# Optimization experiments

Measured on AMD Instinct MI355X. Metric: run time of the kernel, lower is better.

## Reference

```python
import jax, jax.numpy as jnp
import numpy as np

B, S, D = 2, 2048, 1024
H, E = 16, 64          # n_heads, head_dim
DFF = 4096             # intermediate
R_ATTN, R_OUT, R_FF = 32, 512, 512
LN_EPS = 1e-5
SCALE = 1.0 / np.sqrt(E)


def setup_inputs() -> dict:
    key = jax.random.key(0)
    ks = jax.random.split(key, 24)
    s = 0.02
    inp = {
        "hidden_states": jax.random.normal(ks[0], (B, S, D), jnp.float32),
        "ln1_w": jnp.ones((D,), jnp.float32),
        "ln1_b": jnp.zeros((D,), jnp.float32),
        "q_U": jax.random.normal(ks[1], (H, E, R_ATTN), jnp.float32) * s,
        "q_V": jax.random.normal(ks[2], (H, R_ATTN, D), jnp.float32) * s,
        "q_bias": jax.random.normal(ks[3], (H, E), jnp.float32) * s,
        "k_U": jax.random.normal(ks[4], (H, E, R_ATTN), jnp.float32) * s,
        "k_V": jax.random.normal(ks[5], (H, R_ATTN, D), jnp.float32) * s,
        "k_bias": jax.random.normal(ks[6], (H, E), jnp.float32) * s,
        "v_U": jax.random.normal(ks[7], (H, E, R_ATTN), jnp.float32) * s,
        "v_V": jax.random.normal(ks[8], (H, R_ATTN, D), jnp.float32) * s,
        "v_bias": jax.random.normal(ks[9], (H, E), jnp.float32) * s,
        "out_U": jax.random.normal(ks[10], (D, R_OUT), jnp.float32) * s,
        "out_V": jax.random.normal(ks[11], (R_OUT, D), jnp.float32) * s,
        "out_bias": jnp.zeros((D,), jnp.float32),
        "ln2_w": jnp.ones((D,), jnp.float32),
        "ln2_b": jnp.zeros((D,), jnp.float32),
        "fc1_U": jax.random.normal(ks[12], (DFF, R_FF), jnp.float32) * s,
        "fc1_V": jax.random.normal(ks[13], (R_FF, D), jnp.float32) * s,
        "fc1_bias": jnp.zeros((DFF,), jnp.float32),
        "fc2_U": jax.random.normal(ks[14], (D, R_FF), jnp.float32) * s,
        "fc2_V": jax.random.normal(ks[15], (R_FF, DFF), jnp.float32) * s,
        "fc2_bias": jnp.zeros((D,), jnp.float32),
    }
    return inp


def _layernorm(x, w, b):
    mu = jnp.mean(x, axis=-1, keepdims=True)
    var = jnp.mean(jnp.square(x - mu), axis=-1, keepdims=True)
    return (x - mu) * jax.lax.rsqrt(var + LN_EPS) * w + b


def _per_head_svd(x, U, V, bias):
    # x: [b,s,d]; V: [h,r,d]; U: [h,e,r]; bias: [h,e] -> [b,h,s,e]
    t = jnp.einsum("bsd,hrd->bhsr", x, V)
    return jnp.einsum("bhsr,her->bhse", t, U) + bias[None, :, None, :]


def reference(hidden_states, ln1_w, ln1_b, q_U, q_V, q_bias, k_U, k_V, k_bias,
              v_U, v_V, v_bias, out_U, out_V, out_bias, ln2_w, ln2_b,
              fc1_U, fc1_V, fc1_bias, fc2_U, fc2_V, fc2_bias):
    b, s, d = hidden_states.shape
    normed = _layernorm(hidden_states, ln1_w, ln1_b)

    q = _per_head_svd(normed, q_U, q_V, q_bias)  # [b,h,s,e]
    k = _per_head_svd(normed, k_U, k_V, k_bias)
    v = _per_head_svd(normed, v_U, v_V, v_bias)

    scores = jnp.einsum("bhqe,bhke->bhqk", q, k) * SCALE
    causal = jnp.tril(jnp.ones((s, s), dtype=bool))
    scores = jnp.where(causal, scores, -jnp.inf)
    probs = jax.nn.softmax(scores, axis=-1)
    attn = jnp.einsum("bhqk,bhke->bhqe", probs, v)
    attn = attn.transpose(0, 2, 1, 3).reshape(b, s, d)  # [b,s,d]

    attn = jnp.einsum("bsr,dr->bsd", jnp.einsum("bsd,rd->bsr", attn, out_V), out_U) + out_bias
    hidden_states = hidden_states + attn

    normed = _layernorm(hidden_states, ln2_w, ln2_b)
    ff = jnp.einsum("bsr,fr->bsf", jnp.einsum("bsd,rd->bsr", normed, fc1_V), fc1_U) + fc1_bias
    ff = jax.nn.gelu(ff, approximate=False)  # exact erf gelu as in torch F.gelu
    ff = jnp.einsum("bsr,dr->bsd", jnp.einsum("bsf,rf->bsr", ff, fc2_V), fc2_U) + fc2_bias
    hidden_states = hidden_states + ff
    return (hidden_states,)
```

## Files before the change

### kernel.cpp

```cpp
#include <hip/hip_runtime.h>
#include <hip/hip_bf16.h>
#include <math.h>

#define Bc 2
#define Sc 2048
#define Dc 1024
#define Hc 16
#define Ec 64
#define DFFc 4096
#define SCALEc 0.125f
#define SCLOG2E 0.18033688f
#define LN_EPSc 1e-5f
#define BH_STRIDE 131072

typedef short bf16x8 __attribute__((ext_vector_type(8)));
typedef unsigned short u16x4 __attribute__((ext_vector_type(4)));
typedef unsigned short u16x8 __attribute__((ext_vector_type(8)));
typedef float f32x4 __attribute__((ext_vector_type(4)));
typedef float f32x16 __attribute__((ext_vector_type(16)));
typedef unsigned int u32x4 __attribute__((ext_vector_type(4)));
#define MFMA16(a, b, c) __builtin_amdgcn_mfma_f32_16x16x32_bf16(a, b, c, 0, 0, 0)
#define MFMA32(a, b, c) __builtin_amdgcn_mfma_f32_32x32x16_bf16(a, b, c, 0, 0, 0)
#define GLDS16(g, l)                                                            \
  __builtin_amdgcn_global_load_lds((const __attribute__((address_space(1))) void*)(g), \
                                   (__attribute__((address_space(3))) void*)(l), 16, 0, 0)

static __device__ __forceinline__ unsigned short f2bf(float x) {
  unsigned u = __float_as_uint(x);
  unsigned r = (u + 0x7FFFu + ((u >> 16) & 1u)) >> 16;
  return (unsigned short)r;
}
static __device__ __forceinline__ unsigned cvtpk(float lo, float hi) {
  unsigned r;
  asm("v_cvt_pk_bf16_f32 %0, %1, %2" : "=v"(r) : "v"(lo), "v"(hi));
  return r;
}

__global__ __launch_bounds__(256) void prep(
    const float* __restrict__ s3, const float* __restrict__ s4, const float* __restrict__ s5,
    const float* __restrict__ s6, const float* __restrict__ s7, const float* __restrict__ s8,
    unsigned short* __restrict__ wsu,
    const float* __restrict__ x, const float* __restrict__ lw, const float* __restrict__ lb,
    unsigned short* __restrict__ nout,
    const float* __restrict__ qB, const float* __restrict__ kB, const float* __restrict__ vB,
    float* __restrict__ biasF) {
  __shared__ float sm[8];
  int tid = threadIdx.x;
  if (blockIdx.x < 6144) {
    int i = (blockIdx.x * 256 + tid) * 4;
    const float* s;
    int off;
    if (i < 1572864) {
      int seg = i >> 19;
      off = i & 524287;
      s = (seg == 0) ? s3 : (seg == 1) ? s4 : s5;
    } else if (i < 3670016) { s = s6; off = i - 1572864; }
    else if (i < 5767168)   { s = s7; off = i - 3670016; }
    else                    { s = s8; off = i - 5767168; }
    float4 v = *(const float4*)(s + off);
    u16x4 o = {f2bf(v.x), f2bf(v.y), f2bf(v.z), f2bf(v.w)};
    *(u16x4*)(wsu + 1572864 + i) = o;
    return;
  }
  if (blockIdx.x >= 6144 + 4096) {
    int k = blockIdx.x - 6144 - 4096;
    const float* src = (k == 0) ? qB : (k == 1) ? kB : vB;
    float sc = (k == 0) ? SCLOG2E : 1.0f;
    int i = tid * 4;
    float4 v = *(const float4*)(src + i);
    float4 o = {v.x * sc, v.y * sc, v.z * sc, v.w * sc};
    *(float4*)(biasF + k * 1024 + i) = o;
    return;
  }
  int row = blockIdx.x - 6144;
  const float* xr = x + (size_t)row * Dc;
  float v[4];
  float sum = 0.f;
#pragma unroll
  for (int i = 0; i < 4; ++i) { v[i] = xr[tid + i * 256]; sum += v[i]; }
#pragma unroll
  for (int off = 32; off > 0; off >>= 1) sum += __shfl_down(sum, off, 64);
  if ((tid & 63) == 0) sm[tid >> 6] = sum;
  __syncthreads();
  float mean = (sm[0] + sm[1] + sm[2] + sm[3]) * (1.f / Dc);
  float var = 0.f;
#pragma unroll
  for (int i = 0; i < 4; ++i) { float d0 = v[i] - mean; var += d0 * d0; }
#pragma unroll
  for (int off = 32; off > 0; off >>= 1) var += __shfl_down(var, off, 64);
  if ((tid & 63) == 0) sm[4 + (tid >> 6)] = var;
  __syncthreads();
  float rstd = rsqrtf((sm[4] + sm[5] + sm[6] + sm[7]) * (1.f / Dc) + LN_EPSc);
  unsigned short* orow = nout + (size_t)row * Dc;
#pragma unroll
  for (int i = 0; i < 4; ++i) {
    int c = tid + i * 256;
    orow[c] = f2bf((v[i] - mean) * rstd * lw[c] + lb[c]);
  }
}

__global__ __launch_bounds__(256) void makew(const float* __restrict__ qU,
                                             const float* __restrict__ kU,
                                             const float* __restrict__ vU,
                                             const float* __restrict__ qV,
                                             const float* __restrict__ kV,
                                             const float* __restrict__ vV,
                                             unsigned short* __restrict__ W) {
  int bid = blockIdx.x;
  int kind = bid >> 8;
  int h = (bid >> 4) & 15;
  int dblk = bid & 15;
  const float* U = (kind == 0) ? qU : (kind == 1) ? kU : vU;
  const float* V = (kind == 0) ? qV : (kind == 1) ? kV : vV;
  __shared__ float Us[64][33];
  __shared__ float Vs[32][64];
  int tid = threadIdx.x;
  for (int i = tid; i < 2048; i += 256) Us[i >> 5][i & 31] = U[h * 2048 + i];
  for (int i = tid; i < 2048; i += 256) {
    int r = i >> 6, d = i & 63;
    Vs[r][d] = V[h * 32768 + r * 1024 + dblk * 64 + d];
  }
  __syncthreads();
  int e = tid & 63;
  int dq = tid >> 6;
  float scale = (kind == 0) ? SCLOG2E : 1.0f;
  float acc[16] = {};
  for (int r = 0; r < 32; ++r) {
    float u = Us[e][r];
#pragma unroll
    for (int j = 0; j < 16; ++j) acc[j] += u * Vs[r][dq * 16 + j];
  }
  u16x8 o0, o1;
#pragma unroll
  for (int j = 0; j < 8; ++j) {
    o0[j] = f2bf(acc[j] * scale);
    o1[j] = f2bf(acc[8 + j] * scale);
  }
  size_t base = ((size_t)(kind * 1024 + h * 64 + e)) * 1024 + dblk * 64 + dq * 16;
  *(u16x8*)(W + base) = o0;
  *(u16x8*)(W + base + 8) = o1;
}

__global__ __launch_bounds__(256) void ln_bf16(const float* __restrict__ x,
                                               const float* __restrict__ w,
                                               const float* __restrict__ b,
                                               unsigned short* __restrict__ out) {
  __shared__ float sm[8];
  int row = blockIdx.x;
  int tid = threadIdx.x;
  const float* xr = x + (size_t)row * Dc;
  float v[4];
  float sum = 0.f;
#pragma unroll
  for (int i = 0; i < 4; ++i) { v[i] = xr[tid + i * 256]; sum += v[i]; }
#pragma unroll
  for (int off = 32; off > 0; off >>= 1) sum += __shfl_down(sum, off, 64);
  if ((tid & 63) == 0) sm[tid >> 6] = sum;
  __syncthreads();
  float mean = (sm[0] + sm[1] + sm[2] + sm[3]) * (1.f / Dc);
  float var = 0.f;
#pragma unroll
  for (int i = 0; i < 4; ++i) { float d0 = v[i] - mean; var += d0 * d0; }
#pragma unroll
  for (int off = 32; off > 0; off >>= 1) var += __shfl_down(var, off, 64);
  if ((tid & 63) == 0) sm[4 + (tid >> 6)] = var;
  __syncthreads();
  float rstd = rsqrtf((sm[4] + sm[5] + sm[6] + sm[7]) * (1.f / Dc) + LN_EPSc);
  unsigned short* orow = out + (size_t)row * Dc;
#pragma unroll
  for (int i = 0; i < 4; ++i) {
    int c = tid + i * 256;
    orow[c] = f2bf((v[i] - mean) * rstd * w[c] + b[c]);
  }
}

template <int BM, int BN>
__global__ __launch_bounds__(256) void gemm_bf16(const unsigned short* __restrict__ A,
                                                 const unsigned short* __restrict__ W,
                                                 float* __restrict__ Cf,
                                                 unsigned short* __restrict__ Cb,
                                                 const float* __restrict__ bias,
                                                 const float* __restrict__ res,
                                                 int M, int N, int K, int gelu, int nbm) {
  constexpr int BK = 64;
  constexpr int MT = BM / 32;
  constexpr int NT = BN / 32;
  __shared__ unsigned short As[2][BM * BK];
  __shared__ unsigned short Bs[2][BN * BK];
  int tid = threadIdx.x;
  int lane = tid & 63;
  int wid = tid >> 6;
  int cl = lane & 15, grp = lane >> 4;
  int wr = wid >> 1, wc = wid & 1;
  int bm = blockIdx.x % nbm;
  int bn = blockIdx.x / nbm;
  const unsigned short* Ab = A + (size_t)(bm * BM) * K;
  const unsigned short* Wb = W + (size_t)(bn * BN) * K;
  f32x4 acc[MT][NT];
  f32x4 z4 = {0.f, 0.f, 0.f, 0.f};
#pragma unroll
  for (int i = 0; i < MT; ++i)
#pragma unroll
    for (int j = 0; j < NT; ++j) acc[i][j] = z4;
  int r0 = tid >> 3;
  int c0 = (tid & 7) * 8;

#define STAGE(buf, k0)                                                         \
  {                                                                            \
    _Pragma("unroll") for (int l = 0; l < BM / 32; ++l) {                      \
      int row = r0 + l * 32;                                                   \
      int sc = c0 ^ ((row & 7) * 8);                                           \
      GLDS16(Ab + (size_t)row * K + (k0) + sc, &As[buf][(tid + l * 256) * 8]); \
    }                                                                          \
    _Pragma("unroll") for (int l = 0; l < BN / 32; ++l) {                      \
      int row = r0 + l * 32;                                                   \
      int sc = c0 ^ ((row & 7) * 8);                                           \
      GLDS16(Wb + (size_t)row * K + (k0) + sc, &Bs[buf][(tid + l * 256) * 8]); \
    }                                                                          \
  }

  int nt = K / BK;
  STAGE(0, 0)
  __syncthreads();
  for (int t = 0; t < nt; ++t) {
    int cur = t & 1;
    if (t + 1 < nt) STAGE(cur ^ 1, (t + 1) * BK)
#pragma unroll
    for (int kk = 0; kk < 2; ++kk) {
      bf16x8 af[MT], bfr[NT];
#pragma unroll
      for (int i = 0; i < MT; ++i) {
        int row = wr * (BM / 2) + i * 16 + cl;
        af[i] = *(const bf16x8*)&As[cur][row * BK + ((kk * 32 + grp * 8) ^ ((row & 7) * 8))];
      }
#pragma unroll
      for (int j = 0; j < NT; ++j) {
        int row = wc * (BN / 2) + j * 16 + cl;
        bfr[j] = *(const bf16x8*)&Bs[cur][row * BK + ((kk * 32 + grp * 8) ^ ((row & 7) * 8))];
      }
#pragma unroll
      for (int i = 0; i < MT; ++i)
#pragma unroll
        for (int j = 0; j < NT; ++j) acc[i][j] = MFMA16(af[i], bfr[j], acc[i][j]);
    }
    __syncthreads();
  }
#undef STAGE

#pragma unroll
  for (int i = 0; i < MT; ++i) {
    int row = bm * BM + wr * (BM / 2) + i * 16 + grp * 4;
#pragma unroll
    for (int j = 0; j < NT; ++j) {
      int col = bn * BN + wc * (BN / 2) + j * 16 + cl;
      float bv = bias ? bias[col] : 0.f;
#pragma unroll
      for (int r = 0; r < 4; ++r) {
        float v = acc[i][j][r] + bv;
        if (gelu) v = 0.5f * v * (1.f + erff(v * 0.70710678118f));
        if (res) v += res[(size_t)(row + r) * N + col];
        if (Cb) Cb[(size_t)(row + r) * N + col] = f2bf(v);
        else Cf[(size_t)(row + r) * N + col] = v;
      }
    }
  }
}

__global__ __launch_bounds__(256) void gemm_qkv(const unsigned short* __restrict__ A,
                                                const unsigned short* __restrict__ W,
                                                const float* __restrict__ bias,
                                                unsigned short* __restrict__ qO,
                                                unsigned short* __restrict__ kO,
                                                unsigned short* __restrict__ vO,
                                                int K, int nbm) {
  constexpr int BM = 128, BN = 64, BK = 64;
  constexpr int MT = BM / 32;
  constexpr int NT = BN / 32;
  const int N = 3072;
  __shared__ unsigned short As[2][BM * BK];
  __shared__ unsigned short Bs[2][BN * BK];
  int tid = threadIdx.x;
  int lane = tid & 63;
  int wid = tid >> 6;
  int cl = lane & 15, grp = lane >> 4;
  int wr = wid >> 1, wc = wid & 1;
  int bm = blockIdx.x % nbm;
  int bn = blockIdx.x / nbm;
  const unsigned short* Ab = A + (size_t)(bm * BM) * K;
  const unsigned short* Wb = W + (size_t)(bn * BN) * K;
  f32x4 acc[MT][NT];
  f32x4 z4 = {0.f, 0.f, 0.f, 0.f};
#pragma unroll
  for (int i = 0; i < MT; ++i)
#pragma unroll
    for (int j = 0; j < NT; ++j) acc[i][j] = z4;
  int r0 = tid >> 3;
  int c0 = (tid & 7) * 8;

#define STAGE(buf, k0)                                                         \
  {                                                                            \
    _Pragma("unroll") for (int l = 0; l < BM / 32; ++l) {                      \
      int row = r0 + l * 32;                                                   \
      int sc = c0 ^ ((row & 7) * 8);                                           \
      GLDS16(Ab + (size_t)row * K + (k0) + sc, &As[buf][(tid + l * 256) * 8]); \
    }                                                                          \
    _Pragma("unroll") for (int l = 0; l < BN / 32; ++l) {                      \
      int row = r0 + l * 32;                                                   \
      int sc = c0 ^ ((row & 7) * 8);                                           \
      GLDS16(Wb + (size_t)row * K + (k0) + sc, &Bs[buf][(tid + l * 256) * 8]); \
    }                                                                          \
  }

  int nt = K / BK;
  STAGE(0, 0)
  __syncthreads();
  for (int t = 0; t < nt; ++t) {
    int cur = t & 1;
    if (t + 1 < nt) STAGE(cur ^ 1, (t + 1) * BK)
#pragma unroll
    for (int kk = 0; kk < 2; ++kk) {
      bf16x8 af[MT], bfr[NT];
#pragma unroll
      for (int i = 0; i < MT; ++i) {
        int row = wr * (BM / 2) + i * 16 + cl;
        af[i] = *(const bf16x8*)&As[cur][row * BK + ((kk * 32 + grp * 8) ^ ((row & 7) * 8))];
      }
#pragma unroll
      for (int j = 0; j < NT; ++j) {
        int row = wc * (BN / 2) + j * 16 + cl;
        bfr[j] = *(const bf16x8*)&Bs[cur][row * BK + ((kk * 32 + grp * 8) ^ ((row & 7) * 8))];
      }
#pragma unroll
      for (int i = 0; i < MT; ++i)
#pragma unroll
        for (int j = 0; j < NT; ++j) acc[i][j] = MFMA16(af[i], bfr[j], acc[i][j]);
    }
    __syncthreads();
  }
#undef STAGE

#pragma unroll
  for (int i = 0; i < MT; ++i) {
    int row0 = bm * BM + wr * (BM / 2) + i * 16 + grp * 4;
#pragma unroll
    for (int j = 0; j < NT; ++j) {
      int col = bn * BN + wc * (BN / 2) + j * 16 + cl;
      float bv = bias[col];
      int kind = col >> 10;
      int c1 = col & 1023;
      int h = c1 >> 6;
      int e = c1 & 63;
#pragma unroll
      for (int r = 0; r < 4; ++r) {
        int row = row0 + r;
        unsigned short hv = f2bf(acc[i][j][r] + bv);
        int b = row >> 11;
        int rs = row & 2047;
        int sb = rs >> 5;
        int bh = b * Hc + h;
        if (kind < 2) {
          int s = rs & 31;
          int ec = e >> 3;
          int jj = e & 7;
          int es = ec >> 1, hi2 = ec & 1;
          int lanep = s + hi2 * 32;
          unsigned short* out = (kind == 0) ? qO : kO;
          out[(size_t)bh * BH_STRIDE + (size_t)((sb * 4 + es) * 64 + lanep) * 8 + jj] = hv;
        } else {
          int within = rs & 31;
          int sg = within >> 3;
          int si = within & 7;
          int eo = e >> 5, llp = e & 31;
          int h2 = sg >> 1, hi2 = sg & 1;
          int ix = eo * 2 + h2;
          int lanep = llp + hi2 * 32;
          vO[(size_t)bh * BH_STRIDE + (size_t)((sb * 4 + ix) * 64 + lanep) * 8 + si] = hv;
        }
      }
    }
  }
}

template <int BM, int BN>
__global__ __launch_bounds__(256) void gemm_splitk2(const unsigned short* __restrict__ A,
                                                    const unsigned short* __restrict__ W,
                                                    float* __restrict__ P0,
                                                    float* __restrict__ P1,
                                                    int M, int N, int K, int nbm) {
  constexpr int BK = 64;
  constexpr int MT = BM / 32;
  constexpr int NT = BN / 32;
  __shared__ unsigned short As[2][BM * BK];
  __shared__ unsigned short Bs[2][BN * BK];
  int tid = threadIdx.x;
  int lane = tid & 63;
  int wid = tid >> 6;
  int cl = lane & 15, grp = lane >> 4;
  int wr = wid >> 1, wc = wid & 1;
  int per = nbm * (N / BN);
  int slice = blockIdx.x / per;
  int inner = blockIdx.x % per;
  int bm = inner % nbm;
  int bn = inner / nbm;
  int Ks = K / 2;
  const unsigned short* Ab = A + (size_t)(bm * BM) * K + (size_t)slice * Ks;
  const unsigned short* Wb = W + (size_t)(bn * BN) * K + (size_t)slice * Ks;
  float* P = slice ? P1 : P0;
  f32x4 acc[MT][NT];
  f32x4 z4 = {0.f, 0.f, 0.f, 0.f};
#pragma unroll
  for (int i = 0; i < MT; ++i)
#pragma unroll
    for (int j = 0; j < NT; ++j) acc[i][j] = z4;
  int r0 = tid >> 3;
  int c0 = (tid & 7) * 8;

#define STAGE(buf, k0)                                                         \
  {                                                                            \
    _Pragma("unroll") for (int l = 0; l < BM / 32; ++l) {                      \
      int row = r0 + l * 32;                                                   \
      int sc = c0 ^ ((row & 7) * 8);                                           \
      GLDS16(Ab + (size_t)row * K + (k0) + sc, &As[buf][(tid + l * 256) * 8]); \
    }                                                                          \
    _Pragma("unroll") for (int l = 0; l < BN / 32; ++l) {                      \
      int row = r0 + l * 32;                                                   \
      int sc = c0 ^ ((row & 7) * 8);                                           \
      GLDS16(Wb + (size_t)row * K + (k0) + sc, &Bs[buf][(tid + l * 256) * 8]); \
    }                                                                          \
  }

  int nt = Ks / BK;
  STAGE(0, 0)
  __syncthreads();
  for (int t = 0; t < nt; ++t) {
    int cur = t & 1;
    if (t + 1 < nt) STAGE(cur ^ 1, (t + 1) * BK)
#pragma unroll
    for (int kk = 0; kk < 2; ++kk) {
      bf16x8 af[MT], bfr[NT];
#pragma unroll
      for (int i = 0; i < MT; ++i) {
        int row = wr * (BM / 2) + i * 16 + cl;
        af[i] = *(const bf16x8*)&As[cur][row * BK + ((kk * 32 + grp * 8) ^ ((row & 7) * 8))];
      }
#pragma unroll
      for (int j = 0; j < NT; ++j) {
        int row = wc * (BN / 2) + j * 16 + cl;
        bfr[j] = *(const bf16x8*)&Bs[cur][row * BK + ((kk * 32 + grp * 8) ^ ((row & 7) * 8))];
      }
#pragma unroll
      for (int i = 0; i < MT; ++i)
#pragma unroll
        for (int j = 0; j < NT; ++j) acc[i][j] = MFMA16(af[i], bfr[j], acc[i][j]);
    }
    __syncthreads();
  }
#undef STAGE

#pragma unroll
  for (int i = 0; i < MT; ++i) {
    int row = bm * BM + wr * (BM / 2) + i * 16 + grp * 4;
#pragma unroll
    for (int j = 0; j < NT; ++j) {
      int col = bn * BN + wc * (BN / 2) + j * 16 + cl;
#pragma unroll
      for (int r = 0; r < 4; ++r)
        P[(size_t)(row + r) * N + col] = acc[i][j][r];
    }
  }
}

__global__ __launch_bounds__(256) void reduce2(const float* __restrict__ P0,
                                               const float* __restrict__ P1,
                                               unsigned short* __restrict__ out, int n) {
  int i = (blockIdx.x * 256 + threadIdx.x) * 4;
  if (i >= n) return;
  float4 a = *(const float4*)(P0 + i);
  float4 b = *(const float4*)(P1 + i);
  u16x4 o = {f2bf(a.x + b.x), f2bf(a.y + b.y), f2bf(a.z + b.z), f2bf(a.w + b.w)};
  *(u16x4*)(out + i) = o;
}

__global__ __launch_bounds__(256) void attn_mfma(const unsigned short* __restrict__ qf_,
                                                 const unsigned short* __restrict__ kf_,
                                                 const unsigned short* __restrict__ vf_,
                                                 unsigned short* __restrict__ out) {
  __shared__ float MS[2][33][64];
  int tid = threadIdx.x;
  int wid = tid >> 6;
  int lane = tid & 63;
  int ll = lane & 31;
  int hi = lane >> 5;
  int bid = blockIdx.x;
  int xcd = bid & 7;
  int idx = bid >> 3;
  int qt = 63 - (idx >> 2);
  int bh = xcd + 8 * (idx & 3);
  int b = bh >> 4, h = bh & 15;
  const unsigned short* qb = qf_ + (size_t)bh * BH_STRIDE;
  const unsigned short* kb = kf_ + (size_t)bh * BH_STRIDE;
  const unsigned short* vb = vf_ + (size_t)bh * BH_STRIDE;
  int q0 = qt * 32;
  int nt = qt + 1;
  int full = nt - 1;
  int fs = wid * full / 4;
  int fe = (wid + 1) * full / 4;

  bf16x8 qf[4];
#pragma unroll
  for (int es = 0; es < 4; ++es)
    qf[es] = *(const bf16x8*)(qb + (size_t)((qt * 4 + es) * 64 + lane) * 8);

  f32x16 accO[2] = {};
  f32x16 lacc = {};

  int t = fs;
  for (; t + 1 < fe; t += 2) {
    bf16x8 ka[4], kb2[4];
#pragma unroll
    for (int es = 0; es < 4; ++es) {
      ka[es] = *(const bf16x8*)(kb + (size_t)((t * 4 + es) * 64 + lane) * 8);
      kb2[es] = *(const bf16x8*)(kb + (size_t)(((t + 1) * 4 + es) * 64 + lane) * 8);
    }
    f32x16 cA = {}, cB = {};
    __builtin_amdgcn_s_setprio(1);
    cA = MFMA32(ka[0], qf[0], cA);
    cA = MFMA32(ka[1], qf[1], cA);
    cA = MFMA32(ka[2], qf[2], cA);
    cA = MFMA32(ka[3], qf[3], cA);
    cB = MFMA32(kb2[0], qf[0], cB);
    cB = MFMA32(kb2[1], qf[1], cB);
    cB = MFMA32(kb2[2], qf[2], cB);
    cB = MFMA32(kb2[3], qf[3], cB);
    __builtin_amdgcn_s_setprio(0);
    float pA[16], pB[16];
#pragma unroll
    for (int r = 0; r < 16; ++r) { pA[r] = exp2f(cA[r]); pB[r] = exp2f(cB[r]); }
#pragma unroll
    for (int r = 0; r < 16; ++r) lacc[r] += pA[r] + pB[r];
    bf16x8 va[4], vb2[4];
#pragma unroll
    for (int ix = 0; ix < 4; ++ix) {
      va[ix] = *(const bf16x8*)(vb + (size_t)((t * 4 + ix) * 64 + lane) * 8);
      vb2[ix] = *(const bf16x8*)(vb + (size_t)(((t + 1) * 4 + ix) * 64 + lane) * 8);
    }
    unsigned wA0 = cvtpk(pA[0], pA[1]), wA1 = cvtpk(pA[2], pA[3]);
    unsigned wA2 = cvtpk(pA[4], pA[5]), wA3 = cvtpk(pA[6], pA[7]);
    unsigned wA4 = cvtpk(pA[8], pA[9]), wA5 = cvtpk(pA[10], pA[11]);
    unsigned wA6 = cvtpk(pA[12], pA[13]), wA7 = cvtpk(pA[14], pA[15]);
    unsigned wB0 = cvtpk(pB[0], pB[1]), wB1 = cvtpk(pB[2], pB[3]);
    unsigned wB2 = cvtpk(pB[4], pB[5]), wB3 = cvtpk(pB[6], pB[7]);
    unsigned wB4 = cvtpk(pB[8], pB[9]), wB5 = cvtpk(pB[10], pB[11]);
    unsigned wB6 = cvtpk(pB[12], pB[13]), wB7 = cvtpk(pB[14], pB[15]);
    asm("v_permlane32_swap_b32 %0, %1" : "+v"(wA0), "+v"(wA2));
    asm("v_permlane32_swap_b32 %0, %1" : "+v"(wA1), "+v"(wA3));
    asm("v_permlane32_swap_b32 %0, %1" : "+v"(wA4), "+v"(wA6));
    asm("v_permlane32_swap_b32 %0, %1" : "+v"(wA5), "+v"(wA7));
    asm("v_permlane32_swap_b32 %0, %1" : "+v"(wB0), "+v"(wB2));
    asm("v_permlane32_swap_b32 %0, %1" : "+v"(wB1), "+v"(wB3));
    asm("v_permlane32_swap_b32 %0, %1" : "+v"(wB4), "+v"(wB6));
    asm("v_permlane32_swap_b32 %0, %1" : "+v"(wB5), "+v"(wB7));
    u32x4 pA0v = {wA0, wA1, wA2, wA3}, pA1v = {wA4, wA5, wA6, wA7};
    u32x4 pB0v = {wB0, wB1, wB2, wB3}, pB1v = {wB4, wB5, wB6, wB7};
    bf16x8 bA0 = __builtin_bit_cast(bf16x8, pA0v), bA1 = __builtin_bit_cast(bf16x8, pA1v);
    bf16x8 bB0 = __builtin_bit_cast(bf16x8, pB0v), bB1 = __builtin_bit_cast(bf16x8, pB1v);
    __builtin_amdgcn_s_setprio(1);
    accO[0] = MFMA32(va[0], bA0, accO[0]);
    accO[0] = MFMA32(va[1], bA1, accO[0]);
    accO[0] = MFMA32(vb2[0], bB0, accO[0]);
    accO[0] = MFMA32(vb2[1], bB1, accO[0]);
    accO[1] = MFMA32(va[2], bA0, accO[1]);
    accO[1] = MFMA32(va[3], bA1, accO[1]);
    accO[1] = MFMA32(vb2[2], bB0, accO[1]);
    accO[1] = MFMA32(vb2[3], bB1, accO[1]);
    __builtin_amdgcn_s_setprio(0);
  }

#define ATT_ONE(T, MASKED)                                                          \
  {                                                                                 \
    bf16x8 kf1[4];                                                                  \
    _Pragma("unroll") for (int es = 0; es < 4; ++es)                                \
      kf1[es] = *(const bf16x8*)(kb + (size_t)(((T) * 4 + es) * 64 + lane) * 8);    \
    f32x16 c = {};                                                                  \
    __builtin_amdgcn_s_setprio(1);                                                  \
    c = MFMA32(kf1[0], qf[0], c);                                                   \
    c = MFMA32(kf1[1], qf[1], c);                                                   \
    c = MFMA32(kf1[2], qf[2], c);                                                   \
    c = MFMA32(kf1[3], qf[3], c);                                                   \
    __builtin_amdgcn_s_setprio(0);                                                  \
    float p1[16];                                                                   \
    _Pragma("unroll") for (int r = 0; r < 16; ++r) {                                \
      if (MASKED) {                                                                 \
        int keyloc = (r & 3) + 8 * (r >> 2) + 4 * hi;                               \
        p1[r] = (keyloc > ll) ? 0.f : exp2f(c[r]);                                  \
      } else p1[r] = exp2f(c[r]);                                                   \
    }                                                                               \
    _Pragma("unroll") for (int r = 0; r < 16; ++r) lacc[r] += p1[r];                \
    bf16x8 vf1[4];                                                                  \
    _Pragma("unroll") for (int ix = 0; ix < 4; ++ix)                                \
      vf1[ix] = *(const bf16x8*)(vb + (size_t)(((T) * 4 + ix) * 64 + lane) * 8);    \
    unsigned w0 = cvtpk(p1[0], p1[1]), w1 = cvtpk(p1[2], p1[3]);                    \
    unsigned w2 = cvtpk(p1[4], p1[5]), w3 = cvtpk(p1[6], p1[7]);                    \
    unsigned w4 = cvtpk(p1[8], p1[9]), w5 = cvtpk(p1[10], p1[11]);                  \
    unsigned w6 = cvtpk(p1[12], p1[13]), w7 = cvtpk(p1[14], p1[15]);                \
    asm("v_permlane32_swap_b32 %0, %1" : "+v"(w0), "+v"(w2));                       \
    asm("v_permlane32_swap_b32 %0, %1" : "+v"(w1), "+v"(w3));                       \
    asm("v_permlane32_swap_b32 %0, %1" : "+v"(w4), "+v"(w6));                       \
    asm("v_permlane32_swap_b32 %0, %1" : "+v"(w5), "+v"(w7));                       \
    u32x4 pw0 = {w0, w1, w2, w3};                                                   \
    u32x4 pw1 = {w4, w5, w6, w7};                                                   \
    bf16x8 pb0 = __builtin_bit_cast(bf16x8, pw0);                                   \
    bf16x8 pb1 = __builtin_bit_cast(bf16x8, pw1);                                   \
    __builtin_amdgcn_s_setprio(1);                                                  \
    accO[0] = MFMA32(vf1[0], pb0, accO[0]);                                         \
    accO[0] = MFMA32(vf1[1], pb1, accO[0]);                                         \
    accO[1] = MFMA32(vf1[2], pb0, accO[1]);                                         \
    accO[1] = MFMA32(vf1[3], pb1, accO[1]);                                         \
    __builtin_amdgcn_s_setprio(0);                                                  \
  }

  if (t < fe) ATT_ONE(t, false)
  if (wid == 3) ATT_ONE(full, true)
#undef ATT_ONE

  float l;
  {
    float s8[8];
#pragma unroll
    for (int r = 0; r < 8; ++r) s8[r] = lacc[r] + lacc[r + 8];
    float s4a = s8[0] + s8[4], s4b = s8[1] + s8[5], s4c = s8[2] + s8[6], s4d = s8[3] + s8[7];
    l = (s4a + s4b) + (s4c + s4d);
  }

  auto publish = [&](int slot) {
#pragma unroll
    for (int r = 0; r < 16; ++r) {
      MS[slot][r][lane] = accO[0][r];
      MS[slot][16 + r][lane] = accO[1][r];
    }
    MS[slot][32][lane] = l;
  };
  auto merge = [&](int slot) {
    l += MS[slot][32][lane];
#pragma unroll
    for (int r = 0; r < 16; ++r) {
      accO[0][r] += MS[slot][r][lane];
      accO[1][r] += MS[slot][16 + r][lane];
    }
  };
  if (wid == 1) publish(0);
  if (wid == 3) publish(1);
  __syncthreads();
  if (wid == 0) merge(0);
  if (wid == 2) merge(1);
  __syncthreads();
  if (wid == 2) publish(0);
  __syncthreads();
  if (wid == 0) {
    merge(0);
    float ltot = l + __shfl_xor(l, 32, 64);
    float inv = 1.f / ltot;
    unsigned short* orow = out + (size_t)(b * Sc + q0 + ll) * Dc + h * Ec;
#pragma unroll
    for (int eo = 0; eo < 2; ++eo)
#pragma unroll
      for (int g = 0; g < 4; ++g) {
        u16x4 o4 = {f2bf(accO[eo][4 * g + 0] * inv), f2bf(accO[eo][4 * g + 1] * inv),
                    f2bf(accO[eo][4 * g + 2] * inv), f2bf(accO[eo][4 * g + 3] * inv)};
        *(u16x4*)(orow + eo * 32 + 8 * g + 4 * hi) = o4;
      }
  }
}

extern "C" void kernel_launch(void* const* d_in, const int* in_sizes, int n_in,
                              void* d_out, int out_size, void* d_ws, size_t ws_size,
                              hipStream_t stream) {
  const float* hidden = (const float*)d_in[0];
  const float* ln1_w = (const float*)d_in[1];
  const float* ln1_b = (const float*)d_in[2];
  const float* q_U = (const float*)d_in[3];
  const float* q_V = (const float*)d_in[4];
  const float* q_bias = (const float*)d_in[5];
  const float* k_U = (const float*)d_in[6];
  const float* k_V = (const float*)d_in[7];
  const float* k_bias = (const float*)d_in[8];
  const float* v_U = (const float*)d_in[9];
  const float* v_V = (const float*)d_in[10];
  const float* v_bias = (const float*)d_in[11];
  const float* out_U = (const float*)d_in[12];
  const float* out_V = (const float*)d_in[13];
  const float* out_bias = (const float*)d_in[14];
  const float* ln2_w = (const float*)d_in[15];
  const float* ln2_b = (const float*)d_in[16];
  const float* fc1_U = (const float*)d_in[17];
  const float* fc1_V = (const float*)d_in[18];
  const float* fc1_bias = (const float*)d_in[19];
  const float* fc2_U = (const float*)d_in[20];
  const float* fc2_V = (const float*)d_in[21];
  const float* fc2_bias = (const float*)d_in[22];
  float* out = (float*)d_out;
  float* ws = (float*)d_ws;
  unsigned short* wsu = (unsigned short*)d_ws;

  unsigned short* wOUTV = wsu + 1572864;
  unsigned short* wOUTU = wsu + 2097152;
  unsigned short* wFC1V = wsu + 2621440;
  unsigned short* wFC1U = wsu + 3145728;
  unsigned short* wFC2V = wsu + 5242880;
  unsigned short* wFC2U = wsu + 7340032;

  float* h1 = ws + 4194304;
  unsigned short* Wqkv = (unsigned short*)(ws + 4194304);
  float* qkv_biasF = ws + 6000000;
  unsigned short* attn_out = (unsigned short*)(ws + 6291456);
  unsigned short* normed = (unsigned short*)(ws + 8388608);
  unsigned short* rbB = (unsigned short*)(ws + 10485760);
  unsigned short* ff = (unsigned short*)(ws + 11534336);
  unsigned short* qbuf = (unsigned short*)(ws + 16777216);
  unsigned short* kbuf = (unsigned short*)(ws + 18874368);
  unsigned short* vtbuf = (unsigned short*)(ws + 20971520);
  float* P0f = ws + 8388608;
  float* P1f = ws + 19922944;
  unsigned short* rbG2 = (unsigned short*)(ws + 10485760);

  const int M = Bc * Sc;
  dim3 blk(256);

  makew<<<768, blk, 0, stream>>>(q_U, k_U, v_U, q_V, k_V, v_V, Wqkv);
  prep<<<6144 + M + 3, blk, 0, stream>>>(out_V, out_U, fc1_V, fc1_U, fc2_V, fc2_U,
                                         wsu, hidden, ln1_w, ln1_b, normed,
                                         q_bias, k_bias, v_bias, qkv_biasF);

  gemm_qkv<<<1536, blk, 0, stream>>>(normed, Wqkv, qkv_biasF, qbuf, kbuf, vtbuf, Dc, 32);

  attn_mfma<<<2048, blk, 0, stream>>>(qbuf, kbuf, vtbuf, attn_out);

  gemm_bf16<64, 32><<<1024, blk, 0, stream>>>(attn_out, wOUTV, nullptr, rbB, nullptr, nullptr,
                                              M, 512, Dc, 0, 64);
  gemm_bf16<64, 64><<<1024, blk, 0, stream>>>(rbB, wOUTU, h1, nullptr, out_bias, hidden,
                                              M, Dc, 512, 0, 64);

  ln_bf16<<<M, blk, 0, stream>>>(h1, ln2_w, ln2_b, normed);
  gemm_bf16<64, 32><<<1024, blk, 0, stream>>>(normed, wFC1V, nullptr, rbB, nullptr, nullptr,
                                              M, 512, Dc, 0, 64);
  gemm_bf16<128, 64><<<2048, blk, 0, stream>>>(rbB, wFC1U, nullptr, ff, fc1_bias, nullptr,
                                               M, DFFc, 512, 1, 32);
  gemm_splitk2<64, 64><<<1024, blk, 0, stream>>>(ff, wFC2V, P0f, P1f, M, 512, DFFc, 64);
  reduce2<<<2048, blk, 0, stream>>>(P0f, P1f, rbG2, M * 512);
  gemm_bf16<64, 64><<<1024, blk, 0, stream>>>(rbG2, wFC2U, out, nullptr, fc2_bias, h1,
                                              M, Dc, 512, 0, 64);
}
```

Baseline: 229.6 us.

## Fold low-rank out-projection into a dense precomputed weight matrix

Precomputes the dense out-projection weight out_U·out_V in bf16 each call, using a new transpose kernel plus a small GEMM. The attention output then goes through a single K=1024 GEMM instead of two chained low-rank GEMMs. This removes one launch and the intermediate rank-512 buffer round-trip, at roughly equal FLOPs plus the weight-build cost and an extra bf16 rounding of the combined weight.

```diff
diff --git a/kernel.cpp b/kernel.cpp
--- a/kernel.cpp
+++ b/kernel.cpp
@@ -99,6 +99,25 @@
   }
 }
 
+__global__ __launch_bounds__(256) void transp(const float* __restrict__ src,
+                                              unsigned short* __restrict__ dst) {
+  __shared__ unsigned short T[64][65];
+  int bi = blockIdx.x & 15;
+  int bj = blockIdx.x >> 4;
+  int tid = threadIdx.x;
+  for (int k = 0; k < 16; ++k) {
+    int row = (tid >> 6) + k * 4;
+    int col = tid & 63;
+    T[row][col] = f2bf(src[(size_t)(bj * 64 + row) * 1024 + bi * 64 + col]);
+  }
+  __syncthreads();
+  for (int k = 0; k < 16; ++k) {
+    int row = (tid >> 6) + k * 4;
+    int col = tid & 63;
+    dst[(size_t)(bi * 64 + row) * 512 + bj * 64 + col] = T[col][row];
+  }
+}
+
 __global__ __launch_bounds__(256) void makew(const float* __restrict__ qU,
                                              const float* __restrict__ kU,
                                              const float* __restrict__ vU,
@@ -276,7 +295,6 @@
   constexpr int BM = 128, BN = 64, BK = 64;
   constexpr int MT = BM / 32;
   constexpr int NT = BN / 32;
-  const int N = 3072;
   __shared__ unsigned short As[2][BM * BK];
   __shared__ unsigned short Bs[2][BN * BK];
   int tid = threadIdx.x;
@@ -702,6 +720,8 @@
   float* ws = (float*)d_ws;
   unsigned short* wsu = (unsigned short*)d_ws;
 
+  unsigned short* WOUT = wsu;
+  unsigned short* wOUTVT = wsu + 1048576;
   unsigned short* wOUTV = wsu + 1572864;
   unsigned short* wOUTU = wsu + 2097152;
   unsigned short* wFC1V = wsu + 2621440;
@@ -726,19 +746,20 @@
   const int M = Bc * Sc;
   dim3 blk(256);
 
+  transp<<<128, blk, 0, stream>>>(out_V, wOUTVT);
   makew<<<768, blk, 0, stream>>>(q_U, k_U, v_U, q_V, k_V, v_V, Wqkv);
   prep<<<6144 + M + 3, blk, 0, stream>>>(out_V, out_U, fc1_V, fc1_U, fc2_V, fc2_U,
                                          wsu, hidden, ln1_w, ln1_b, normed,
                                          q_bias, k_bias, v_bias, qkv_biasF);
+  gemm_bf16<64, 64><<<256, blk, 0, stream>>>(wOUTU, wOUTVT, nullptr, WOUT, nullptr, nullptr,
+                                             1024, 1024, 512, 0, 16);
 
   gemm_qkv<<<1536, blk, 0, stream>>>(normed, Wqkv, qkv_biasF, qbuf, kbuf, vtbuf, Dc, 32);
 
   attn_mfma<<<2048, blk, 0, stream>>>(qbuf, kbuf, vtbuf, attn_out);
 
-  gemm_bf16<64, 32><<<1024, blk, 0, stream>>>(attn_out, wOUTV, nullptr, rbB, nullptr, nullptr,
-                                              M, 512, Dc, 0, 64);
-  gemm_bf16<64, 64><<<1024, blk, 0, stream>>>(rbB, wOUTU, h1, nullptr, out_bias, hidden,
-                                              M, Dc, 512, 0, 64);
+  gemm_bf16<128, 64><<<512, blk, 0, stream>>>(attn_out, WOUT, h1, nullptr, out_bias, hidden,
+                                              M, Dc, Dc, 0, 32);
 
   ln_bf16<<<M, blk, 0, stream>>>(h1, ln2_w, ln2_b, normed);
   gemm_bf16<64, 32><<<1024, blk, 0, stream>>>(normed, wFC1V, nullptr, rbB, nullptr, nullptr,
```

New measurement: 240.6 us. +4.8%, slower.
